# Kernel tuning notes

Measured on AMD Instinct MI355X. Metric: run time of the kernel, lower is better.

## Reference

```python
import jax, jax.numpy as jnp
import numpy as np

DIM = 256; Hh = 64; Ww = 64; L = Hh * Ww; B = 2
DIN = DIM          # expand = 1
DST = 16           # d_state
DTR = 16           # dt_rank = ceil(dim/16)
DCONV = 4


def _ln(x, g, b, eps=1e-5):
    m = jnp.mean(x, -1, keepdims=True)
    v = jnp.mean((x - m) ** 2, -1, keepdims=True)
    return (x - m) / jnp.sqrt(v + eps) * g + b


def _scan_dir(x, ep, z, convW, convb, xpW, dtW, dtb, A_log, Dp):
    # x, ep, z: (B, d_inner, L)
    xc = jnp.pad(x, ((0, 0), (0, 0), (DCONV - 1, 0)))  # causal depthwise conv
    xc = jax.lax.conv_general_dilated(
        xc, convW[:, None, :], (1,), 'VALID',
        feature_group_count=DIN, dimension_numbers=('NCH', 'OIH', 'NCH'))
    xs = jax.nn.silu(xc + convb[None, :, None])
    # cross: dt, B, C come from the OTHER modality's embedding (v7 cross-SSM)
    xdbl = jnp.einsum('bdl,kd->bkl', ep, xpW)               # (B, DTR+2N, L)
    dt = jax.nn.softplus(jnp.einsum('brl,dr->bdl', xdbl[:, :DTR], dtW) + dtb[None, :, None])
    Bm = xdbl[:, DTR:DTR + DST]                             # (B, N, L)
    Cm = xdbl[:, DTR + DST:]                                # (B, N, L)
    A = -jnp.exp(A_log)                                     # (d, N)
    dA = jnp.exp(jnp.einsum('bdl,dn->bdln', dt, A))         # (B, d, L, N)
    dBx = jnp.einsum('bdl,bnl,bdl->bdln', dt, Bm, xs)
    def comb(c1, c2):
        a1, b1 = c1; a2, b2 = c2
        return a1 * a2, a2 * b1 + b2
    _, h = jax.lax.associative_scan(comb, (dA, dBx), axis=2)  # h_l = dA_l h_{l-1} + dBx_l
    y = jnp.einsum('bdln,bnl->bdl', h, Cm) + Dp[None, :, None] * xs
    return y * jax.nn.silu(z)


def _mamba(u, e, in_proj_W, extra_proj_W,
           convf_W, convf_b, xprojf_W, dtf_W, dtf_b, A_log_f, D_f,
           convb_W, convb_b, xprojb_W, dtb_W, dtb_b, A_log_b, D_b,
           outnorm_g, outnorm_b, out_proj_W):
    xz = u @ in_proj_W.T                                    # (B, L, 2*d_inner)
    x = xz[..., :DIN].transpose(0, 2, 1)                    # (B, d, L)
    z = xz[..., DIN:].transpose(0, 2, 1)
    ep = (e @ extra_proj_W.T).transpose(0, 2, 1)            # (B, d, L)
    yf = _scan_dir(x, ep, z, convf_W, convf_b, xprojf_W, dtf_W, dtf_b, A_log_f, D_f)
    yb = jnp.flip(_scan_dir(jnp.flip(x, -1), jnp.flip(ep, -1), jnp.flip(z, -1),
                            convb_W, convb_b, xprojb_W, dtb_W, dtb_b, A_log_b, D_b), -1)
    y = (yf + yb) * 0.5                                     # if_devide_out
    y = _ln(y.transpose(0, 2, 1), outnorm_g, outnorm_b)     # use_norm
    return y @ out_proj_W.T


def setup_inputs() -> dict:
    key = jax.random.key(0)
    ks = jax.random.split(key, 20)
    s = 0.05
    dt_bias = float(np.log(np.expm1(0.01)))
    inp = {
        'input0': jax.random.normal(ks[0], (B, L, DIM), jnp.float32),
        'input1': jax.random.normal(ks[1], (B, L, DIM), jnp.float32),
        'norm0_g': jnp.ones((DIM,), jnp.float32), 'norm0_b': jnp.zeros((DIM,), jnp.float32),
        'norm1_g': jnp.ones((DIM,), jnp.float32), 'norm1_b': jnp.zeros((DIM,), jnp.float32),
        'cw_W': jax.random.normal(ks[2], (DIM, 2 * DIM), jnp.float32) * s,
        'cw_b': jnp.zeros((DIM,), jnp.float32),
        'in_proj_W': jax.random.normal(ks[3], (2 * DIN, DIM), jnp.float32) * s,
        'extra_proj_W': jax.random.normal(ks[4], (DIN, DIM), jnp.float32) * s,
        'convf_W': jax.random.normal(ks[5], (DIN, DCONV), jnp.float32) * 0.3,
        'convf_b': jnp.zeros((DIN,), jnp.float32),
        'xprojf_W': jax.random.normal(ks[6], (DTR + 2 * DST, DIN), jnp.float32) * s,
        'dtf_W': jax.random.normal(ks[7], (DIN, DTR), jnp.float32) * s,
        'dtf_b': jnp.full((DIN,), dt_bias, jnp.float32),
        'A_log_f': jnp.broadcast_to(jnp.log(jnp.arange(1, DST + 1, dtype=jnp.float32)), (DIN, DST)).copy(),
        'D_f': jnp.ones((DIN,), jnp.float32),
        'convb_W': jax.random.normal(ks[8], (DIN, DCONV), jnp.float32) * 0.3,
        'convb_b': jnp.zeros((DIN,), jnp.float32),
        'xprojb_W': jax.random.normal(ks[9], (DTR + 2 * DST, DIN), jnp.float32) * s,
        'dtb_W': jax.random.normal(ks[10], (DIN, DTR), jnp.float32) * s,
        'dtb_b': jnp.full((DIN,), dt_bias, jnp.float32),
        'A_log_b': jnp.broadcast_to(jnp.log(jnp.arange(1, DST + 1, dtype=jnp.float32)), (DIN, DST)).copy(),
        'D_b': jnp.ones((DIN,), jnp.float32),
        'outnorm_g': jnp.ones((DIN,), jnp.float32), 'outnorm_b': jnp.zeros((DIN,), jnp.float32),
        'out_proj_W': jax.random.normal(ks[11], (DIM, DIN), jnp.float32) * s,
        'post_g': jnp.ones((DIM,), jnp.float32), 'post_b': jnp.zeros((DIM,), jnp.float32),
    }
    return inp


def reference(input0, input1, norm0_g, norm0_b, norm1_g, norm1_b, cw_W, cw_b,
              in_proj_W, extra_proj_W,
              convf_W, convf_b, xprojf_W, dtf_W, dtf_b, A_log_f, D_f,
              convb_W, convb_b, xprojb_W, dtb_W, dtb_b, A_log_b, D_b,
              outnorm_g, outnorm_b, out_proj_W, post_g, post_b):
    skip = input0
    x0 = _ln(input0, norm0_g, norm0_b)
    x1 = _ln(input1, norm1_g, norm1_b)
    w = jax.nn.sigmoid(jnp.concatenate([x0, x1], -1) @ cw_W.T + cw_b)
    out = _mamba(x0, x1, in_proj_W, extra_proj_W,
                 convf_W, convf_b, xprojf_W, dtf_W, dtf_b, A_log_f, D_f,
                 convb_W, convb_b, xprojb_W, dtb_W, dtb_b, A_log_b, D_b,
                 outnorm_g, outnorm_b, out_proj_W)
    out = _ln(out, post_g, post_b)
    out = out * w + x0 * (1 - w)
    return out + skip
```

## Files before the change

kernel.cpp:

```cpp
#include <hip/hip_runtime.h>
#include <cstddef>

#define LL 4096
#define BB 2
#define DD 256
#define NEL ((size_t)BB * LL * DD)

typedef __bf16 bf16x8 __attribute__((ext_vector_type(8)));
typedef float f32x4 __attribute__((ext_vector_type(4)));
typedef unsigned short u16;

__device__ __forceinline__ float4 ld4(const float* p) { return *reinterpret_cast<const float4*>(p); }
__device__ __forceinline__ void st4(float* p, const float4 v) { *reinterpret_cast<float4*>(p) = v; }
__device__ __forceinline__ float softplusf(float x) { return fmaxf(x, 0.f) + log1pf(expf(-fabsf(x))); }
__device__ __forceinline__ u16 f2b(float f) {
    union { float f; unsigned u; } v; v.f = f;
    unsigned u = v.u;
    return (u16)((u + 0x7fffu + ((u >> 16) & 1u)) >> 16);
}

__device__ __forceinline__ void load16(const float* __restrict__ p, int fwd, float* dst) {
    if (fwd) {
#pragma unroll
        for (int k = 0; k < 4; ++k) {
            float4 v = ld4(p + 4 * k);
            dst[4 * k] = v.x; dst[4 * k + 1] = v.y; dst[4 * k + 2] = v.z; dst[4 * k + 3] = v.w;
        }
    } else {
#pragma unroll
        for (int k = 0; k < 4; ++k) {
            float4 v = ld4(p + 4 * k);
            dst[15 - 4 * k] = v.x; dst[14 - 4 * k] = v.y; dst[13 - 4 * k] = v.z; dst[12 - 4 * k] = v.w;
        }
    }
}

__device__ __forceinline__ void load16s(const float* __restrict__ row, int t, float* dst) {
#pragma unroll
    for (int s4 = 0; s4 < 4; ++s4) {
        float4 v = ld4(row + s4 * 1024 + t * 4);
        dst[4 * s4] = v.x; dst[4 * s4 + 1] = v.y; dst[4 * s4 + 2] = v.z; dst[4 * s4 + 3] = v.w;
    }
}


__global__ __launch_bounds__(256) void prep_q(
    const float* __restrict__ xpf, const float* __restrict__ xpb,
    const float* __restrict__ extW, float* __restrict__ Q, u16* __restrict__ wsH)
{
    const int r = blockIdx.x % 48;
    const int dir = blockIdx.x / 48;
    const int k = threadIdx.x;
    const float* xp = dir ? xpb : xpf;
    float s = 0.f;
    for (int n = 0; n < 256; ++n) s = fmaf(xp[r * 256 + n], extW[n * 256 + k], s);
    if (r < 16) Q[(dir * 16 + r) * 256 + k] = s;
    else        wsH[393216 + ((dir ? 32 : 0) + (r - 16)) * 256 + k] = f2b(s);
}

__global__ __launch_bounds__(256) void prep_w(
    const float* __restrict__ inW, const float* __restrict__ cwW,
    const float* __restrict__ outW, const float* __restrict__ dtfW,
    const float* __restrict__ dtbW, const float* __restrict__ Q,
    u16* __restrict__ wsH)
{
    const int idx = blockIdx.x * 256 + threadIdx.x;
    if (idx < 131072) {
        wsH[idx] = f2b(inW[idx]);
    } else if (idx < 262144) {
        wsH[idx] = f2b(cwW[idx - 131072]);
    } else if (idx < 393216) {
        const int i = idx - 262144;
        const int dir = i >> 16;
        const int j = i & 65535;
        const int n = j >> 8, k = j & 255;
        const float* dtW = dir ? dtbW : dtfW;
        const float* Qd = Q + dir * 4096;
        float s = 0.f;
#pragma unroll
        for (int r = 0; r < 16; ++r) s = fmaf(dtW[n * 16 + r], Qd[r * 256 + k], s);
        wsH[idx] = f2b(s);
    } else if (idx >= 409600 && idx < 475136) {
        wsH[idx] = f2b(outW[idx - 409600]);
    }
}

__global__ __launch_bounds__(64) void ln_rows(
    const float* __restrict__ in, float* __restrict__ outf, u16* __restrict__ outh,
    const float* __restrict__ g, const float* __restrict__ bb)
{
    const int row = blockIdx.x;
    const int t = threadIdx.x;
    const size_t off = (size_t)row * 256 + t * 4;
    float4 v = ld4(&in[off]);
    float s = v.x + v.y + v.z + v.w;
    float s2 = v.x * v.x + v.y * v.y + v.z * v.z + v.w * v.w;
#pragma unroll
    for (int dl = 1; dl < 64; dl <<= 1) { s += __shfl_xor(s, dl); s2 += __shfl_xor(s2, dl); }
    const float m = s * (1.f / 256.f);
    const float var = s2 * (1.f / 256.f) - m * m;
    const float rstd = rsqrtf(var + 1e-5f);
    const float4 gv = ld4(&g[t * 4]);
    const float4 bv = ld4(&bb[t * 4]);
    float4 r;
    r.x = (v.x - m) * rstd * gv.x + bv.x;
    r.y = (v.y - m) * rstd * gv.y + bv.y;
    r.z = (v.z - m) * rstd * gv.z + bv.z;
    r.w = (v.w - m) * rstd * gv.w + bv.w;
    if (outf) st4(&outf[off], r);
    ushort4 h; h.x = f2b(r.x); h.y = f2b(r.y); h.z = f2b(r.z); h.w = f2b(r.w);
    *reinterpret_cast<ushort4*>(&outh[off]) = h;
}

__global__ __launch_bounds__(256) void gemm_mfma(
    const u16* __restrict__ x0h, const u16* __restrict__ x1h, const u16* __restrict__ wsH,
    const float* __restrict__ cwb, const float* __restrict__ dtfb, const float* __restrict__ dtbb,
    float* __restrict__ xT, float* __restrict__ zT, float* __restrict__ wbuf,
    float* __restrict__ dtfT, float* __restrict__ dtbT,
    float* __restrict__ bcfT, float* __restrict__ bcbT)
{
    __shared__ __align__(16) u16 Blds[64 * 256];
    const int t = threadIdx.x;
    const int lane = t & 63;
    const int wid = t >> 6;
    const int col = lane & 15;
    const int kq = lane >> 4;
    const int m0 = blockIdx.x * 128;
    const int by = blockIdx.y;

    int seg, nbase, ldk, nhalf; const u16* W;
    if (by < 4)       { seg = 0; W = wsH + (size_t)(by * 64) * 256;                 ldk = 256; nhalf = 1; nbase = by * 64; }
    else if (by < 8)  { seg = 1; W = wsH + (size_t)(by * 64) * 256;                 ldk = 256; nhalf = 1; nbase = (by - 4) * 64; }
    else if (by < 12) { seg = 2; W = wsH + 131072 + (size_t)((by - 8) * 64) * 512;  ldk = 512; nhalf = 2; nbase = (by - 8) * 64; }
    else if (by < 16) { seg = 3; W = wsH + 262144 + (size_t)((by - 12) * 64) * 256; ldk = 256; nhalf = 1; nbase = (by - 12) * 64; }
    else if (by < 20) { seg = 4; W = wsH + 327680 + (size_t)((by - 16) * 64) * 256; ldk = 256; nhalf = 1; nbase = (by - 16) * 64; }
    else              { seg = 5; W = wsH + 393216;                                  ldk = 256; nhalf = 1; nbase = 0; }

    const u16* A0 = (seg >= 3) ? x1h : x0h;
    const int arow = m0 + wid * 32 + col;

    f32x4 acc[2][4] = {};
    for (int half = 0; half < nhalf; ++half) {
        if (half) __syncthreads();
#pragma unroll
        for (int it = 0; it < 8; ++it) {
            const int c = it * 256 + t;
            const int row = c >> 5, kc = c & 31;
            const bf16x8 v = *reinterpret_cast<const bf16x8*>(W + (size_t)row * ldk + half * 256 + kc * 8);
            const unsigned byt = ((unsigned)(row * 512 + kc * 16)) ^ (((unsigned)row & 7u) << 4);
            *reinterpret_cast<bf16x8*>(reinterpret_cast<char*>(Blds) + byt) = v;
        }
        __syncthreads();
        const u16* Ap = (seg == 2 && half) ? x1h : A0;
        const u16* Abase = Ap + (size_t)arow * 256;
        for (int k0 = 0; k0 < 256; k0 += 32) {
            const int kk = k0 + kq * 8;
            const bf16x8 a0 = *reinterpret_cast<const bf16x8*>(Abase + kk);
            const bf16x8 a1 = *reinterpret_cast<const bf16x8*>(Abase + 16 * 256 + kk);
#pragma unroll
            for (int nf = 0; nf < 4; ++nf) {
                const int n = nf * 16 + col;
                const unsigned byt = ((unsigned)(n * 512 + k0 * 2 + kq * 16)) ^ (((unsigned)n & 7u) << 4);
                const bf16x8 bfr = *reinterpret_cast<const bf16x8*>(reinterpret_cast<const char*>(Blds) + byt);
                acc[0][nf] = __builtin_amdgcn_mfma_f32_16x16x32_bf16(a0, bfr, acc[0][nf], 0, 0, 0);
                acc[1][nf] = __builtin_amdgcn_mfma_f32_16x16x32_bf16(a1, bfr, acc[1][nf], 0, 0, 0);
            }
        }
    }

    const int bb2 = m0 >> 12;
    const int l0 = m0 & (LL - 1);

    if (seg == 0 || seg == 1) {
        float* dst = (seg == 0) ? xT : zT;
#pragma unroll
        for (int rg = 0; rg < 2; ++rg) {
            const int mrow = wid * 32 + rg * 16 + kq * 4;
#pragma unroll
            for (int nf = 0; nf < 4; ++nf) {
                const int d = nbase + nf * 16 + col;
                *reinterpret_cast<f32x4*>(&dst[((size_t)bb2 * DD + d) * LL + l0 + mrow]) = acc[rg][nf];
            }
        }
    } else if (seg == 2) {
#pragma unroll
        for (int rg = 0; rg < 2; ++rg) {
            const int mrow = wid * 32 + rg * 16 + kq * 4;
#pragma unroll
            for (int nf = 0; nf < 4; ++nf) {
                const int n = nbase + nf * 16 + col;
                const float bv = cwb[n];
#pragma unroll
                for (int r = 0; r < 4; ++r)
                    wbuf[(size_t)(m0 + mrow + r) * 256 + n] = 1.f / (1.f + expf(-(acc[rg][nf][r] + bv)));
            }
        }
    } else if (seg == 3 || seg == 4) {
        const float* bias = (seg == 3) ? dtfb : dtbb;
        float* dst = (seg == 3) ? dtfT : dtbT;
#pragma unroll
        for (int rg = 0; rg < 2; ++rg) {
            const int tt = (l0 >> 4) + wid * 2 + rg;
#pragma unroll
            for (int nf = 0; nf < 4; ++nf) {
                const int d = nbase + nf * 16 + col;
                const float bv = bias[d];
                f32x4 o;
#pragma unroll
                for (int r = 0; r < 4; ++r) o[r] = softplusf(acc[rg][nf][r] + bv);
                const size_t rowb = ((size_t)bb2 * DD + d) * LL;
                if (seg == 3) {
                    *reinterpret_cast<f32x4*>(&dst[rowb + kq * 1024 + tt * 4]) = o;
                } else {
                    f32x4 orv = { o[3], o[2], o[1], o[0] };
                    *reinterpret_cast<f32x4*>(&dst[rowb + (3 - kq) * 1024 + (255 - tt) * 4]) = orv;
                }
            }
        }
    } else {
#pragma unroll
        for (int rg = 0; rg < 2; ++rg) {
            const int tt = (l0 >> 4) + wid * 2 + rg;
#pragma unroll
            for (int nf = 0; nf < 4; ++nf) {
                const int n = nf * 16 + col;
                const int comp = n & 31;
                if (n < 32) {
                    const size_t rowb = ((size_t)bb2 * 32 + comp) * LL;
                    *reinterpret_cast<f32x4*>(&bcfT[rowb + kq * 1024 + tt * 4]) = acc[rg][nf];
                } else {
                    const f32x4 a = acc[rg][nf];
                    f32x4 arv = { a[3], a[2], a[1], a[0] };
                    const size_t rowb = ((size_t)bb2 * 32 + comp) * LL;
                    *reinterpret_cast<f32x4*>(&bcbT[rowb + (3 - kq) * 1024 + (255 - tt) * 4]) = arv;
                }
            }
        }
    }
}

__global__ __launch_bounds__(256) void gemm_out_mfma(
    const u16* __restrict__ ynh, const u16* __restrict__ wsH, float* __restrict__ out)
{
    __shared__ __align__(16) u16 Blds[64 * 256];
    const int t = threadIdx.x;
    const int lane = t & 63;
    const int wid = t >> 6;
    const int col = lane & 15;
    const int kq = lane >> 4;
    const int m0 = blockIdx.x * 128;
    const int n0 = blockIdx.y * 64;
    const u16* W = wsH + 409600 + (size_t)n0 * 256;
    const int arow = m0 + wid * 32 + col;

#pragma unroll
    for (int it = 0; it < 8; ++it) {
        const int c = it * 256 + t;
        const int row = c >> 5, kc = c & 31;
        const bf16x8 v = *reinterpret_cast<const bf16x8*>(W + (size_t)row * 256 + kc * 8);
        const unsigned byt = ((unsigned)(row * 512 + kc * 16)) ^ (((unsigned)row & 7u) << 4);
        *reinterpret_cast<bf16x8*>(reinterpret_cast<char*>(Blds) + byt) = v;
    }
    __syncthreads();

    f32x4 acc[2][4] = {};
    const u16* Abase = ynh + (size_t)arow * 256;
    for (int k0 = 0; k0 < 256; k0 += 32) {
        const int kk = k0 + kq * 8;
        const bf16x8 a0 = *reinterpret_cast<const bf16x8*>(Abase + kk);
        const bf16x8 a1 = *reinterpret_cast<const bf16x8*>(Abase + 16 * 256 + kk);
#pragma unroll
        for (int nf = 0; nf < 4; ++nf) {
            const int n = nf * 16 + col;
            const unsigned byt = ((unsigned)(n * 512 + k0 * 2 + kq * 16)) ^ (((unsigned)n & 7u) << 4);
            const bf16x8 bfr = *reinterpret_cast<const bf16x8*>(reinterpret_cast<const char*>(Blds) + byt);
            acc[0][nf] = __builtin_amdgcn_mfma_f32_16x16x32_bf16(a0, bfr, acc[0][nf], 0, 0, 0);
            acc[1][nf] = __builtin_amdgcn_mfma_f32_16x16x32_bf16(a1, bfr, acc[1][nf], 0, 0, 0);
        }
    }
#pragma unroll
    for (int rg = 0; rg < 2; ++rg) {
        const int mrow = wid * 32 + rg * 16 + kq * 4;
#pragma unroll
        for (int nf = 0; nf < 4; ++nf) {
            const int n = n0 + nf * 16 + col;
#pragma unroll
            for (int r = 0; r < 4; ++r)
                out[(size_t)(m0 + mrow + r) * 256 + n] = acc[rg][nf][r];
        }
    }
}

__global__ __launch_bounds__(256) void scan_kernel(
    const float* __restrict__ xT, const float* __restrict__ zT,
    const float* __restrict__ dtfT, const float* __restrict__ dtbT,
    const float* __restrict__ bcfT, const float* __restrict__ bcbT,
    const float* __restrict__ cfW, const float* __restrict__ cfB,
    const float* __restrict__ cbW, const float* __restrict__ cbB,
    const float* __restrict__ AlF, const float* __restrict__ AlB,
    const float* __restrict__ DF, const float* __restrict__ DB,
    float* __restrict__ yF, float* __restrict__ yB)
{
    const int d = blockIdx.x;
    const int b = blockIdx.y;
    const int dir = blockIdx.z;
    const int t = threadIdx.x;
    const int lane = t & 63;
    const int wv = t >> 6;
    const int fwd = (dir == 0);
    const float* dtT = fwd ? dtfT : dtbT;
    const float* bcT = fwd ? bcfT : bcbT;
    const float* cW  = fwd ? cfW  : cbW;
    const float* cBv = fwd ? cfB  : cbB;
    const float* Al  = fwd ? AlF  : AlB;
    const float* Dp  = fwd ? DF   : DB;
    float* yout = fwd ? yF : yB;

    const int p0 = t * 16;
    const size_t xbase = ((size_t)b * DD + d) * LL;
    const int ls = LL - 16 - p0;
    const int off16 = fwd ? p0 : ls;

    const float Dd = Dp[d];
    const float c0 = cW[d * 4 + 0], c1 = cW[d * 4 + 1], c2 = cW[d * 4 + 2], c3 = cW[d * 4 + 3];
    const float cbias = cBv[d];

    float xq[19];
    if (fwd) {
#pragma unroll
        for (int k = 0; k < 4; ++k) {
            float4 v = ld4(&xT[xbase + p0 + 4 * k]);
            xq[3 + 4 * k] = v.x; xq[4 + 4 * k] = v.y; xq[5 + 4 * k] = v.z; xq[6 + 4 * k] = v.w;
        }
        xq[2] = (p0 >= 1) ? xT[xbase + p0 - 1] : 0.f;
        xq[1] = (p0 >= 2) ? xT[xbase + p0 - 2] : 0.f;
        xq[0] = (p0 >= 3) ? xT[xbase + p0 - 3] : 0.f;
    } else {
#pragma unroll
        for (int k = 0; k < 4; ++k) {
            float4 v = ld4(&xT[xbase + ls + 4 * k]);
            xq[18 - 4 * k] = v.x; xq[17 - 4 * k] = v.y; xq[16 - 4 * k] = v.z; xq[15 - 4 * k] = v.w;
        }
        xq[2] = (p0 >= 1) ? xT[xbase + LL - p0] : 0.f;
        xq[1] = (p0 >= 2) ? xT[xbase + LL + 1 - p0] : 0.f;
        xq[0] = (p0 >= 3) ? xT[xbase + LL + 2 - p0] : 0.f;
    }

    float dt[16];
    load16s(dtT + xbase, t, dt);

    float dtxs[16], yacc[16];
#pragma unroll
    for (int s = 0; s < 16; ++s) {
        float c = fmaf(xq[s], c0, fmaf(xq[s + 1], c1, fmaf(xq[s + 2], c2, fmaf(xq[s + 3], c3, cbias))));
        const float xv = c / (1.f + expf(-c));
        dtxs[s] = dt[s] * xv;
        yacc[s] = Dd * xv;
    }

    const float* bcb0 = bcT + (size_t)b * 32 * LL;

    __shared__ float wPs[2][4];
    __shared__ float wSs[2][4];

#pragma unroll 1
    for (int n = 0; n < 16; ++n) {
        const float a2 = -expf(Al[d * 16 + n]) * 1.4426950408889634f;
        float Bn[16];
        load16s(bcb0 + (size_t)n * LL, t, Bn);
        float pw[16], hl[16];
        float Pl = 1.f, Sl = 0.f;
#pragma unroll
        for (int s = 0; s < 16; ++s) {
            const float w = exp2f(dt[s] * a2);
            Sl = fmaf(w, Sl, dtxs[s] * Bn[s]);
            Pl *= w;
            pw[s] = Pl; hl[s] = Sl;
        }
        float Cn[16];
        load16s(bcb0 + (size_t)(16 + n) * LL, t, Cn);
#pragma unroll
        for (int dl = 1; dl < 64; dl <<= 1) {
            const float Pp = __shfl_up(Pl, dl);
            const float Sp = __shfl_up(Sl, dl);
            if (lane >= dl) { Sl = fmaf(Pl, Sp, Sl); Pl *= Pp; }
        }
        const int buf = n & 1;
        if (lane == 63) { wPs[buf][wv] = Pl; wSs[buf][wv] = Sl; }
        __syncthreads();
        float WSv = 0.f;
#pragma unroll
        for (int w2 = 0; w2 < 3; ++w2)
            if (w2 < wv) WSv = fmaf(wPs[buf][w2], WSv, wSs[buf][w2]);
        const float Pex = __shfl_up(Pl, 1);
        const float Sex = __shfl_up(Sl, 1);
        const float hin = lane ? fmaf(Pex, WSv, Sex) : WSv;
#pragma unroll
        for (int s = 0; s < 16; ++s)
            yacc[s] = fmaf(fmaf(pw[s], hin, hl[s]), Cn[s], yacc[s]);
    }

    float zq[16];
    load16(&zT[xbase + off16], fwd, zq);
    float yv[16];
#pragma unroll
    for (int s = 0; s < 16; ++s) {
        const float zz = zq[s];
        yv[s] = yacc[s] * zz / (1.f + expf(-zz));
    }

    if (fwd) {
#pragma unroll
        for (int k = 0; k < 4; ++k)
            st4(&yout[xbase + p0 + 4 * k], make_float4(yv[4 * k], yv[4 * k + 1], yv[4 * k + 2], yv[4 * k + 3]));
    } else {
#pragma unroll
        for (int k = 0; k < 4; ++k)
            st4(&yout[xbase + ls + 4 * k], make_float4(yv[15 - 4 * k], yv[14 - 4 * k], yv[13 - 4 * k], yv[12 - 4 * k]));
    }
}

__global__ __launch_bounds__(256) void comb_ln(
    const float* __restrict__ yF, const float* __restrict__ yB,
    const float* __restrict__ g, const float* __restrict__ bb,
    u16* __restrict__ out)
{
    __shared__ float tile[256][33];
    __shared__ float rs[8][32];
    __shared__ float rs2[8][32];
    const int b = blockIdx.y;
    const int l0 = blockIdx.x * 32;
    const int t = threadIdx.x;
    {
        const size_t base = ((size_t)b * DD + t) * LL + l0;
#pragma unroll
        for (int k = 0; k < 8; ++k) {
            float4 f = ld4(&yF[base + 4 * k]);
            float4 bv = ld4(&yB[base + 4 * k]);
            tile[t][4 * k + 0] = (f.x + bv.x) * 0.5f;
            tile[t][4 * k + 1] = (f.y + bv.y) * 0.5f;
            tile[t][4 * k + 2] = (f.z + bv.z) * 0.5f;
            tile[t][4 * k + 3] = (f.w + bv.w) * 0.5f;
        }
    }
    __syncthreads();
    const int l = t & 31;
    const int grp = t >> 5;
    float s = 0.f, s2 = 0.f;
#pragma unroll
    for (int i = 0; i < 32; ++i) {
        const float v = tile[grp * 32 + i][l];
        s += v; s2 = fmaf(v, v, s2);
    }
    rs[grp][l] = s; rs2[grp][l] = s2;
    __syncthreads();
    float st = 0.f, st2 = 0.f;
#pragma unroll
    for (int gq = 0; gq < 8; ++gq) { st += rs[gq][l]; st2 += rs2[gq][l]; }
    const float m = st * (1.f / 256.f);
    const float var = st2 * (1.f / 256.f) - m * m;
    const float rstd = rsqrtf(var + 1e-5f);
    const size_t obase = ((size_t)b * LL + l0 + l) * 256 + grp * 32;
#pragma unroll
    for (int k = 0; k < 8; ++k) {
        const float4 gv = ld4(&g[grp * 32 + 4 * k]);
        const float4 bv2 = ld4(&bb[grp * 32 + 4 * k]);
        ushort4 h;
        h.x = f2b((tile[grp * 32 + 4 * k + 0][l] - m) * rstd * gv.x + bv2.x);
        h.y = f2b((tile[grp * 32 + 4 * k + 1][l] - m) * rstd * gv.y + bv2.y);
        h.z = f2b((tile[grp * 32 + 4 * k + 2][l] - m) * rstd * gv.z + bv2.z);
        h.w = f2b((tile[grp * 32 + 4 * k + 3][l] - m) * rstd * gv.w + bv2.w);
        *reinterpret_cast<ushort4*>(&out[obase + 4 * k]) = h;
    }
}

__global__ __launch_bounds__(64) void final_kernel(
    const float* __restrict__ o, const float* __restrict__ w,
    const float* __restrict__ x0n, const float* __restrict__ in0,
    const float* __restrict__ pg, const float* __restrict__ pb,
    float* __restrict__ outp)
{
    const int row = blockIdx.x;
    const int t = threadIdx.x;
    const size_t off = (size_t)row * 256 + t * 4;
    float4 v = ld4(&o[off]);
    float s = v.x + v.y + v.z + v.w;
    float s2 = v.x * v.x + v.y * v.y + v.z * v.z + v.w * v.w;
#pragma unroll
    for (int dl = 1; dl < 64; dl <<= 1) { s += __shfl_xor(s, dl); s2 += __shfl_xor(s2, dl); }
    const float m = s * (1.f / 256.f);
    const float var = s2 * (1.f / 256.f) - m * m;
    const float rstd = rsqrtf(var + 1e-5f);
    const float4 gv = ld4(&pg[t * 4]);
    const float4 bv = ld4(&pb[t * 4]);
    const float4 wv = ld4(&w[off]);
    const float4 xv = ld4(&x0n[off]);
    const float4 iv = ld4(&in0[off]);
    float4 r;
    r.x = ((v.x - m) * rstd * gv.x + bv.x) * wv.x + xv.x * (1.f - wv.x) + iv.x;
    r.y = ((v.y - m) * rstd * gv.y + bv.y) * wv.y + xv.y * (1.f - wv.y) + iv.y;
    r.z = ((v.z - m) * rstd * gv.z + bv.z) * wv.z + xv.z * (1.f - wv.z) + iv.z;
    r.w = ((v.w - m) * rstd * gv.w + bv.w) * wv.w + xv.w * (1.f - wv.w) + iv.w;
    st4(&outp[off], r);
}

extern "C" void kernel_launch(void* const* d_in, const int* in_sizes, int n_in,
                              void* d_out, int out_size, void* d_ws, size_t ws_size,
                              hipStream_t stream) {
    (void)in_sizes; (void)n_in; (void)out_size; (void)ws_size;
    const float* in0      = (const float*)d_in[0];
    const float* in1      = (const float*)d_in[1];
    const float* norm0_g  = (const float*)d_in[2];
    const float* norm0_b  = (const float*)d_in[3];
    const float* norm1_g  = (const float*)d_in[4];
    const float* norm1_b  = (const float*)d_in[5];
    const float* cw_W     = (const float*)d_in[6];
    const float* cw_b     = (const float*)d_in[7];
    const float* in_proj_W    = (const float*)d_in[8];
    const float* extra_proj_W = (const float*)d_in[9];
    const float* convf_W  = (const float*)d_in[10];
    const float* convf_b  = (const float*)d_in[11];
    const float* xprojf_W = (const float*)d_in[12];
    const float* dtf_W    = (const float*)d_in[13];
    const float* dtf_b    = (const float*)d_in[14];
    const float* A_log_f  = (const float*)d_in[15];
    const float* D_f      = (const float*)d_in[16];
    const float* convb_W  = (const float*)d_in[17];
    const float* convb_b  = (const float*)d_in[18];
    const float* xprojb_W = (const float*)d_in[19];
    const float* dtb_W    = (const float*)d_in[20];
    const float* dtb_b    = (const float*)d_in[21];
    const float* A_log_b  = (const float*)d_in[22];
    const float* D_b      = (const float*)d_in[23];
    const float* outnorm_g = (const float*)d_in[24];
    const float* outnorm_b = (const float*)d_in[25];
    const float* out_proj_W = (const float*)d_in[26];
    const float* post_g   = (const float*)d_in[27];
    const float* post_b   = (const float*)d_in[28];

    float* ws = (float*)d_ws;
    float* x0n   = ws;
    float* xT    = ws + NEL;
    float* zT    = ws + 2 * NEL;
    float* dtfT  = ws + 3 * NEL;
    float* dtbT  = ws + 4 * NEL;
    float* wbuf  = ws + 5 * NEL;
    float* yF    = ws + 6 * NEL;
    float* yB    = ws + 7 * NEL;
    float* bcfT  = ws + 8 * NEL;
    float* bcbT  = bcfT + (size_t)BB * 32 * LL;
    u16*   wsH   = (u16*)(bcbT + (size_t)BB * 32 * LL);
    float* Qtmp  = (float*)(wsH + 475136);

    u16* x0h = (u16*)yF;
    u16* x1h = x0h + NEL;
    u16* ynormh = (u16*)dtfT;
    float* obuf = dtbT;

    prep_q<<<96, 256, 0, stream>>>(xprojf_W, xprojb_W, extra_proj_W, Qtmp, wsH);
    prep_w<<<1856, 256, 0, stream>>>(in_proj_W, cw_W, out_proj_W, dtf_W, dtb_W, Qtmp, wsH);
    ln_rows<<<BB * LL, 64, 0, stream>>>(in0, x0n, x0h, norm0_g, norm0_b);
    ln_rows<<<BB * LL, 64, 0, stream>>>(in1, nullptr, x1h, norm1_g, norm1_b);
    gemm_mfma<<<dim3(64, 21, 1), 256, 0, stream>>>(x0h, x1h, wsH, cw_b, dtf_b, dtb_b,
                                                   xT, zT, wbuf, dtfT, dtbT, bcfT, bcbT);
    scan_kernel<<<dim3(256, 2, 2), 256, 0, stream>>>(xT, zT, dtfT, dtbT, bcfT, bcbT,
                                                     convf_W, convf_b, convb_W, convb_b,
                                                     A_log_f, A_log_b, D_f, D_b,
                                                     yF, yB);
    comb_ln<<<dim3(128, 2, 1), 256, 0, stream>>>(yF, yB, outnorm_g, outnorm_b, ynormh);
    gemm_out_mfma<<<dim3(64, 4, 1), 256, 0, stream>>>(ynormh, wsH, obuf);
    final_kernel<<<BB * LL, 64, 0, stream>>>(obuf, wbuf, x0n, in0, post_g, post_b, (float*)d_out);
}
```

Measured before the change: 125.1 us.

## Split scan sequence across 512 threads with 8 elements per thread

The selective-scan kernel now runs 512 threads per block, each handling 8 sequence positions instead of 16. The permuted dt/B/C loads are remapped so each thread takes half of its former owner's chunk, and the cross-wave carry combine is extended from 4 to 8 waves. The goal is a shorter per-thread serial recurrence, fewer registers per thread and more parallelism to hide latency. In exchange, each block does more shuffle-scan and cross-wave combine work.

```diff
diff --git a/kernel.cpp b/kernel.cpp
--- a/kernel.cpp
+++ b/kernel.cpp
@@ -35,11 +35,13 @@
     }
 }
 
-__device__ __forceinline__ void load16s(const float* __restrict__ row, int t, float* dst) {
-#pragma unroll
-    for (int s4 = 0; s4 < 4; ++s4) {
-        float4 v = ld4(row + s4 * 1024 + t * 4);
-        dst[4 * s4] = v.x; dst[4 * s4 + 1] = v.y; dst[4 * s4 + 2] = v.z; dst[4 * s4 + 3] = v.w;
+__device__ __forceinline__ void load8s(const float* __restrict__ row, int t, float* dst) {
+    const int tt = t >> 1;
+    const int s4b = (t & 1) * 2;
+#pragma unroll
+    for (int q = 0; q < 2; ++q) {
+        float4 v = ld4(row + (s4b + q) * 1024 + tt * 4);
+        dst[4 * q] = v.x; dst[4 * q + 1] = v.y; dst[4 * q + 2] = v.z; dst[4 * q + 3] = v.w;
     }
 }
 
@@ -291,7 +293,7 @@
     }
 }
 
-__global__ __launch_bounds__(256) void scan_kernel(
+__global__ __launch_bounds__(512) void scan_kernel(
     const float* __restrict__ xT, const float* __restrict__ zT,
     const float* __restrict__ dtfT, const float* __restrict__ dtbT,
     const float* __restrict__ bcfT, const float* __restrict__ bcbT,
@@ -316,19 +318,18 @@
     const float* Dp  = fwd ? DF   : DB;
     float* yout = fwd ? yF : yB;
 
-    const int p0 = t * 16;
+    const int p0 = t * 8;
     const size_t xbase = ((size_t)b * DD + d) * LL;
-    const int ls = LL - 16 - p0;
-    const int off16 = fwd ? p0 : ls;
+    const int ls = LL - 8 - p0;
 
     const float Dd = Dp[d];
     const float c0 = cW[d * 4 + 0], c1 = cW[d * 4 + 1], c2 = cW[d * 4 + 2], c3 = cW[d * 4 + 3];
     const float cbias = cBv[d];
 
-    float xq[19];
+    float xq[11];
     if (fwd) {
 #pragma unroll
-        for (int k = 0; k < 4; ++k) {
+        for (int k = 0; k < 2; ++k) {
             float4 v = ld4(&xT[xbase + p0 + 4 * k]);
             xq[3 + 4 * k] = v.x; xq[4 + 4 * k] = v.y; xq[5 + 4 * k] = v.z; xq[6 + 4 * k] = v.w;
         }
@@ -337,21 +338,21 @@
         xq[0] = (p0 >= 3) ? xT[xbase + p0 - 3] : 0.f;
     } else {
 #pragma unroll
-        for (int k = 0; k < 4; ++k) {
+        for (int k = 0; k < 2; ++k) {
             float4 v = ld4(&xT[xbase + ls + 4 * k]);
-            xq[18 - 4 * k] = v.x; xq[17 - 4 * k] = v.y; xq[16 - 4 * k] = v.z; xq[15 - 4 * k] = v.w;
+            xq[10 - 4 * k] = v.x; xq[9 - 4 * k] = v.y; xq[8 - 4 * k] = v.z; xq[7 - 4 * k] = v.w;
         }
         xq[2] = (p0 >= 1) ? xT[xbase + LL - p0] : 0.f;
         xq[1] = (p0 >= 2) ? xT[xbase + LL + 1 - p0] : 0.f;
         xq[0] = (p0 >= 3) ? xT[xbase + LL + 2 - p0] : 0.f;
     }
 
-    float dt[16];
-    load16s(dtT + xbase, t, dt);
-
-    float dtxs[16], yacc[16];
-#pragma unroll
-    for (int s = 0; s < 16; ++s) {
+    float dt[8];
+    load8s(dtT + xbase, t, dt);
+
+    float dtxs[8], yacc[8];
+#pragma unroll
+    for (int s = 0; s < 8; ++s) {
         float c = fmaf(xq[s], c0, fmaf(xq[s + 1], c1, fmaf(xq[s + 2], c2, fmaf(xq[s + 3], c3, cbias))));
         const float xv = c / (1.f + expf(-c));
         dtxs[s] = dt[s] * xv;
@@ -360,25 +361,25 @@
 
     const float* bcb0 = bcT + (size_t)b * 32 * LL;
 
-    __shared__ float wPs[2][4];
-    __shared__ float wSs[2][4];
+    __shared__ float wPs[2][8];
+    __shared__ float wSs[2][8];
 
 #pragma unroll 1
     for (int n = 0; n < 16; ++n) {
         const float a2 = -expf(Al[d * 16 + n]) * 1.4426950408889634f;
-        float Bn[16];
-        load16s(bcb0 + (size_t)n * LL, t, Bn);
-        float pw[16], hl[16];
+        float Bn[8];
+        load8s(bcb0 + (size_t)n * LL, t, Bn);
+        float pw[8], hl[8];
         float Pl = 1.f, Sl = 0.f;
 #pragma unroll
-        for (int s = 0; s < 16; ++s) {
+        for (int s = 0; s < 8; ++s) {
             const float w = exp2f(dt[s] * a2);
             Sl = fmaf(w, Sl, dtxs[s] * Bn[s]);
             Pl *= w;
             pw[s] = Pl; hl[s] = Sl;
         }
-        float Cn[16];
-        load16s(bcb0 + (size_t)(16 + n) * LL, t, Cn);
+        float Cn[8];
+        load8s(bcb0 + (size_t)(16 + n) * LL, t, Cn);
 #pragma unroll
         for (int dl = 1; dl < 64; dl <<= 1) {
             const float Pp = __shfl_up(Pl, dl);
@@ -390,33 +391,45 @@
         __syncthreads();
         float WSv = 0.f;
 #pragma unroll
-        for (int w2 = 0; w2 < 3; ++w2)
+        for (int w2 = 0; w2 < 7; ++w2)
             if (w2 < wv) WSv = fmaf(wPs[buf][w2], WSv, wSs[buf][w2]);
         const float Pex = __shfl_up(Pl, 1);
         const float Sex = __shfl_up(Sl, 1);
         const float hin = lane ? fmaf(Pex, WSv, Sex) : WSv;
 #pragma unroll
-        for (int s = 0; s < 16; ++s)
+        for (int s = 0; s < 8; ++s)
             yacc[s] = fmaf(fmaf(pw[s], hin, hl[s]), Cn[s], yacc[s]);
     }
 
-    float zq[16];
-    load16(&zT[xbase + off16], fwd, zq);
-    float yv[16];
-#pragma unroll
-    for (int s = 0; s < 16; ++s) {
+    float zq[8];
+    if (fwd) {
+#pragma unroll
+        for (int k = 0; k < 2; ++k) {
+            float4 v = ld4(&zT[xbase + p0 + 4 * k]);
+            zq[4 * k] = v.x; zq[4 * k + 1] = v.y; zq[4 * k + 2] = v.z; zq[4 * k + 3] = v.w;
+        }
+    } else {
+#pragma unroll
+        for (int k = 0; k < 2; ++k) {
+            float4 v = ld4(&zT[xbase + ls + 4 * k]);
+            zq[7 - 4 * k] = v.x; zq[6 - 4 * k] = v.y; zq[5 - 4 * k] = v.z; zq[4 - 4 * k] = v.w;
+        }
+    }
+    float yv[8];
+#pragma unroll
+    for (int s = 0; s < 8; ++s) {
         const float zz = zq[s];
         yv[s] = yacc[s] * zz / (1.f + expf(-zz));
     }
 
     if (fwd) {
 #pragma unroll
-        for (int k = 0; k < 4; ++k)
+        for (int k = 0; k < 2; ++k)
             st4(&yout[xbase + p0 + 4 * k], make_float4(yv[4 * k], yv[4 * k + 1], yv[4 * k + 2], yv[4 * k + 3]));
     } else {
 #pragma unroll
-        for (int k = 0; k < 4; ++k)
-            st4(&yout[xbase + ls + 4 * k], make_float4(yv[15 - 4 * k], yv[14 - 4 * k], yv[13 - 4 * k], yv[12 - 4 * k]));
+        for (int k = 0; k < 2; ++k)
+            st4(&yout[xbase + ls + 4 * k], make_float4(yv[7 - 4 * k], yv[6 - 4 * k], yv[5 - 4 * k], yv[4 - 4 * k]));
     }
 }
 
@@ -563,7 +576,7 @@
     ln_rows<<<BB * LL, 64, 0, stream>>>(in1, nullptr, x1h, norm1_g, norm1_b);
     gemm_mfma<<<dim3(64, 21, 1), 256, 0, stream>>>(x0h, x1h, wsH, cw_b, dtf_b, dtb_b,
                                                    xT, zT, wbuf, dtfT, dtbT, bcfT, bcbT);
-    scan_kernel<<<dim3(256, 2, 2), 256, 0, stream>>>(xT, zT, dtfT, dtbT, bcfT, bcbT,
+    scan_kernel<<<dim3(256, 2, 2), 512, 0, stream>>>(xT, zT, dtfT, dtbT, bcfT, bcbT,
                                                      convf_W, convf_b, convb_W, convb_b,
                                                      A_log_f, A_log_b, D_f, D_b,
                                                      yF, yB);
```

New measurement: 133.8 us. 1.07x slower.

## Store x, z and scan outputs in bf16; fuse LN launches and recompute x0 norm

Applied to the files above, without the earlier changes.

The x and z projections and the forward/backward scan outputs are now stored as bf16 instead of fp32, which halves the intermediate traffic between the GEMM, the scan and comb_ln. The two layernorm launches are merged into one kernel. The fp32 x0 normalised buffer is no longer written; the final kernel recomputes LN(input0) instead. The C-row load in the scan is hoisted next to the B load. Lower precision in x, z and y adds rounding error in exchange for less memory traffic.

```diff
diff --git a/kernel.cpp b/kernel.cpp
--- a/kernel.cpp
+++ b/kernel.cpp
@@ -18,20 +18,29 @@
     unsigned u = v.u;
     return (u16)((u + 0x7fffu + ((u >> 16) & 1u)) >> 16);
 }
-
-__device__ __forceinline__ void load16(const float* __restrict__ p, int fwd, float* dst) {
+__device__ __forceinline__ float b2f(unsigned bits16) {
+    union { unsigned u; float f; } v; v.u = bits16 << 16; return v.f;
+}
+
+__device__ __forceinline__ void load16h(const u16* __restrict__ p, int fwd, float* dst) {
+    const uint4 a = *reinterpret_cast<const uint4*>(p);
+    const uint4 c = *reinterpret_cast<const uint4*>(p + 8);
+    const unsigned* au = reinterpret_cast<const unsigned*>(&a);
+    const unsigned* cu = reinterpret_cast<const unsigned*>(&c);
+    float tmp[16];
+#pragma unroll
+    for (int j = 0; j < 4; ++j) {
+        tmp[2 * j]     = b2f(au[j] & 0xffffu);
+        tmp[2 * j + 1] = b2f(au[j] >> 16);
+        tmp[8 + 2 * j]     = b2f(cu[j] & 0xffffu);
+        tmp[8 + 2 * j + 1] = b2f(cu[j] >> 16);
+    }
     if (fwd) {
 #pragma unroll
-        for (int k = 0; k < 4; ++k) {
-            float4 v = ld4(p + 4 * k);
-            dst[4 * k] = v.x; dst[4 * k + 1] = v.y; dst[4 * k + 2] = v.z; dst[4 * k + 3] = v.w;
-        }
+        for (int s = 0; s < 16; ++s) dst[s] = tmp[s];
     } else {
 #pragma unroll
-        for (int k = 0; k < 4; ++k) {
-            float4 v = ld4(p + 4 * k);
-            dst[15 - 4 * k] = v.x; dst[14 - 4 * k] = v.y; dst[13 - 4 * k] = v.z; dst[12 - 4 * k] = v.w;
-        }
+        for (int s = 0; s < 16; ++s) dst[s] = tmp[15 - s];
     }
 }
 
@@ -85,11 +94,18 @@
     }
 }
 
-__global__ __launch_bounds__(64) void ln_rows(
-    const float* __restrict__ in, float* __restrict__ outf, u16* __restrict__ outh,
-    const float* __restrict__ g, const float* __restrict__ bb)
-{
-    const int row = blockIdx.x;
+__global__ __launch_bounds__(64) void ln_rows2(
+    const float* __restrict__ in0, const float* __restrict__ in1,
+    const float* __restrict__ g0, const float* __restrict__ b0,
+    const float* __restrict__ g1, const float* __restrict__ b1,
+    u16* __restrict__ x0h, u16* __restrict__ x1h)
+{
+    const int which = blockIdx.x >> 13;
+    const int row = blockIdx.x & 8191;
+    const float* in = which ? in1 : in0;
+    const float* g  = which ? g1 : g0;
+    const float* bb = which ? b1 : b0;
+    u16* outh = which ? x1h : x0h;
     const int t = threadIdx.x;
     const size_t off = (size_t)row * 256 + t * 4;
     float4 v = ld4(&in[off]);
@@ -102,20 +118,18 @@
     const float rstd = rsqrtf(var + 1e-5f);
     const float4 gv = ld4(&g[t * 4]);
     const float4 bv = ld4(&bb[t * 4]);
-    float4 r;
-    r.x = (v.x - m) * rstd * gv.x + bv.x;
-    r.y = (v.y - m) * rstd * gv.y + bv.y;
-    r.z = (v.z - m) * rstd * gv.z + bv.z;
-    r.w = (v.w - m) * rstd * gv.w + bv.w;
-    if (outf) st4(&outf[off], r);
-    ushort4 h; h.x = f2b(r.x); h.y = f2b(r.y); h.z = f2b(r.z); h.w = f2b(r.w);
+    ushort4 h;
+    h.x = f2b((v.x - m) * rstd * gv.x + bv.x);
+    h.y = f2b((v.y - m) * rstd * gv.y + bv.y);
+    h.z = f2b((v.z - m) * rstd * gv.z + bv.z);
+    h.w = f2b((v.w - m) * rstd * gv.w + bv.w);
     *reinterpret_cast<ushort4*>(&outh[off]) = h;
 }
 
 __global__ __launch_bounds__(256) void gemm_mfma(
     const u16* __restrict__ x0h, const u16* __restrict__ x1h, const u16* __restrict__ wsH,
     const float* __restrict__ cwb, const float* __restrict__ dtfb, const float* __restrict__ dtbb,
-    float* __restrict__ xT, float* __restrict__ zT, float* __restrict__ wbuf,
+    u16* __restrict__ xTh, u16* __restrict__ zTh, float* __restrict__ wbuf,
     float* __restrict__ dtfT, float* __restrict__ dtbT,
     float* __restrict__ bcfT, float* __restrict__ bcbT)
 {
@@ -172,14 +186,17 @@
     const int l0 = m0 & (LL - 1);
 
     if (seg == 0 || seg == 1) {
-        float* dst = (seg == 0) ? xT : zT;
+        u16* dst = (seg == 0) ? xTh : zTh;
 #pragma unroll
         for (int rg = 0; rg < 2; ++rg) {
             const int mrow = wid * 32 + rg * 16 + kq * 4;
 #pragma unroll
             for (int nf = 0; nf < 4; ++nf) {
                 const int d = nbase + nf * 16 + col;
-                *reinterpret_cast<f32x4*>(&dst[((size_t)bb2 * DD + d) * LL + l0 + mrow]) = acc[rg][nf];
+                ushort4 h;
+                h.x = f2b(acc[rg][nf][0]); h.y = f2b(acc[rg][nf][1]);
+                h.z = f2b(acc[rg][nf][2]); h.w = f2b(acc[rg][nf][3]);
+                *reinterpret_cast<ushort4*>(&dst[((size_t)bb2 * DD + d) * LL + l0 + mrow]) = h;
             }
         }
     } else if (seg == 2) {
@@ -292,14 +309,14 @@
 }
 
 __global__ __launch_bounds__(256) void scan_kernel(
-    const float* __restrict__ xT, const float* __restrict__ zT,
+    const u16* __restrict__ xTh, const u16* __restrict__ zTh,
     const float* __restrict__ dtfT, const float* __restrict__ dtbT,
     const float* __restrict__ bcfT, const float* __restrict__ bcbT,
     const float* __restrict__ cfW, const float* __restrict__ cfB,
     const float* __restrict__ cbW, const float* __restrict__ cbB,
     const float* __restrict__ AlF, const float* __restrict__ AlB,
     const float* __restrict__ DF, const float* __restrict__ DB,
-    float* __restrict__ yF, float* __restrict__ yB)
+    u16* __restrict__ yFh, u16* __restrict__ yBh)
 {
     const int d = blockIdx.x;
     const int b = blockIdx.y;
@@ -314,7 +331,7 @@
     const float* cBv = fwd ? cfB  : cbB;
     const float* Al  = fwd ? AlF  : AlB;
     const float* Dp  = fwd ? DF   : DB;
-    float* yout = fwd ? yF : yB;
+    u16* yout = fwd ? yFh : yBh;
 
     const int p0 = t * 16;
     const size_t xbase = ((size_t)b * DD + d) * LL;
@@ -326,24 +343,15 @@
     const float cbias = cBv[d];
 
     float xq[19];
+    load16h(&xTh[xbase + off16], fwd, xq + 3);
     if (fwd) {
-#pragma unroll
-        for (int k = 0; k < 4; ++k) {
-            float4 v = ld4(&xT[xbase + p0 + 4 * k]);
-            xq[3 + 4 * k] = v.x; xq[4 + 4 * k] = v.y; xq[5 + 4 * k] = v.z; xq[6 + 4 * k] = v.w;
-        }
-        xq[2] = (p0 >= 1) ? xT[xbase + p0 - 1] : 0.f;
-        xq[1] = (p0 >= 2) ? xT[xbase + p0 - 2] : 0.f;
-        xq[0] = (p0 >= 3) ? xT[xbase + p0 - 3] : 0.f;
+        xq[2] = (p0 >= 1) ? b2f(xTh[xbase + p0 - 1]) : 0.f;
+        xq[1] = (p0 >= 2) ? b2f(xTh[xbase + p0 - 2]) : 0.f;
+        xq[0] = (p0 >= 3) ? b2f(xTh[xbase + p0 - 3]) : 0.f;
     } else {
-#pragma unroll
-        for (int k = 0; k < 4; ++k) {
-            float4 v = ld4(&xT[xbase + ls + 4 * k]);
-            xq[18 - 4 * k] = v.x; xq[17 - 4 * k] = v.y; xq[16 - 4 * k] = v.z; xq[15 - 4 * k] = v.w;
-        }
-        xq[2] = (p0 >= 1) ? xT[xbase + LL - p0] : 0.f;
-        xq[1] = (p0 >= 2) ? xT[xbase + LL + 1 - p0] : 0.f;
-        xq[0] = (p0 >= 3) ? xT[xbase + LL + 2 - p0] : 0.f;
+        xq[2] = (p0 >= 1) ? b2f(xTh[xbase + LL - p0]) : 0.f;
+        xq[1] = (p0 >= 2) ? b2f(xTh[xbase + LL + 1 - p0]) : 0.f;
+        xq[0] = (p0 >= 3) ? b2f(xTh[xbase + LL + 2 - p0]) : 0.f;
     }
 
     float dt[16];
@@ -366,8 +374,9 @@
 #pragma unroll 1
     for (int n = 0; n < 16; ++n) {
         const float a2 = -expf(Al[d * 16 + n]) * 1.4426950408889634f;
-        float Bn[16];
+        float Bn[16], Cn[16];
         load16s(bcb0 + (size_t)n * LL, t, Bn);
+        load16s(bcb0 + (size_t)(16 + n) * LL, t, Cn);
         float pw[16], hl[16];
         float Pl = 1.f, Sl = 0.f;
 #pragma unroll
@@ -377,8 +386,6 @@
             Pl *= w;
             pw[s] = Pl; hl[s] = Sl;
         }
-        float Cn[16];
-        load16s(bcb0 + (size_t)(16 + n) * LL, t, Cn);
 #pragma unroll
         for (int dl = 1; dl < 64; dl <<= 1) {
             const float Pp = __shfl_up(Pl, dl);
@@ -401,7 +408,7 @@
     }
 
     float zq[16];
-    load16(&zT[xbase + off16], fwd, zq);
+    load16h(&zTh[xbase + off16], fwd, zq);
     float yv[16];
 #pragma unroll
     for (int s = 0; s < 16; ++s) {
@@ -409,19 +416,26 @@
         yv[s] = yacc[s] * zz / (1.f + expf(-zz));
     }
 
-    if (fwd) {
-#pragma unroll
-        for (int k = 0; k < 4; ++k)
-            st4(&yout[xbase + p0 + 4 * k], make_float4(yv[4 * k], yv[4 * k + 1], yv[4 * k + 2], yv[4 * k + 3]));
-    } else {
-#pragma unroll
-        for (int k = 0; k < 4; ++k)
-            st4(&yout[xbase + ls + 4 * k], make_float4(yv[15 - 4 * k], yv[14 - 4 * k], yv[13 - 4 * k], yv[12 - 4 * k]));
+#pragma unroll
+    for (int g = 0; g < 2; ++g) {
+        uint4 U;
+        unsigned* up = reinterpret_cast<unsigned*>(&U);
+        if (fwd) {
+#pragma unroll
+            for (int j = 0; j < 4; ++j)
+                up[j] = (unsigned)f2b(yv[8 * g + 2 * j]) | ((unsigned)f2b(yv[8 * g + 2 * j + 1]) << 16);
+            *reinterpret_cast<uint4*>(&yout[xbase + p0 + 8 * g]) = U;
+        } else {
+#pragma unroll
+            for (int j = 0; j < 4; ++j)
+                up[j] = (unsigned)f2b(yv[15 - 8 * g - 2 * j]) | ((unsigned)f2b(yv[15 - 8 * g - 2 * j - 1]) << 16);
+            *reinterpret_cast<uint4*>(&yout[xbase + ls + 8 * g]) = U;
+        }
     }
 }
 
 __global__ __launch_bounds__(256) void comb_ln(
-    const float* __restrict__ yF, const float* __restrict__ yB,
+    const u16* __restrict__ yFh, const u16* __restrict__ yBh,
     const float* __restrict__ g, const float* __restrict__ bb,
     u16* __restrict__ out)
 {
@@ -434,13 +448,16 @@
     {
         const size_t base = ((size_t)b * DD + t) * LL + l0;
 #pragma unroll
-        for (int k = 0; k < 8; ++k) {
-            float4 f = ld4(&yF[base + 4 * k]);
-            float4 bv = ld4(&yB[base + 4 * k]);
-            tile[t][4 * k + 0] = (f.x + bv.x) * 0.5f;
-            tile[t][4 * k + 1] = (f.y + bv.y) * 0.5f;
-            tile[t][4 * k + 2] = (f.z + bv.z) * 0.5f;
-            tile[t][4 * k + 3] = (f.w + bv.w) * 0.5f;
+        for (int k = 0; k < 4; ++k) {
+            const uint4 fa = *reinterpret_cast<const uint4*>(&yFh[base + 8 * k]);
+            const uint4 ba = *reinterpret_cast<const uint4*>(&yBh[base + 8 * k]);
+            const unsigned* fu = reinterpret_cast<const unsigned*>(&fa);
+            const unsigned* bu = reinterpret_cast<const unsigned*>(&ba);
+#pragma unroll
+            for (int j = 0; j < 4; ++j) {
+                tile[t][8 * k + 2 * j]     = (b2f(fu[j] & 0xffffu) + b2f(bu[j] & 0xffffu)) * 0.5f;
+                tile[t][8 * k + 2 * j + 1] = (b2f(fu[j] >> 16) + b2f(bu[j] >> 16)) * 0.5f;
+            }
         }
     }
     __syncthreads();
@@ -476,7 +493,8 @@
 
 __global__ __launch_bounds__(64) void final_kernel(
     const float* __restrict__ o, const float* __restrict__ w,
-    const float* __restrict__ x0n, const float* __restrict__ in0,
+    const float* __restrict__ in0,
+    const float* __restrict__ n0g, const float* __restrict__ n0b,
     const float* __restrict__ pg, const float* __restrict__ pb,
     float* __restrict__ outp)
 {
@@ -484,23 +502,34 @@
     const int t = threadIdx.x;
     const size_t off = (size_t)row * 256 + t * 4;
     float4 v = ld4(&o[off]);
+    float4 iv = ld4(&in0[off]);
     float s = v.x + v.y + v.z + v.w;
     float s2 = v.x * v.x + v.y * v.y + v.z * v.z + v.w * v.w;
-#pragma unroll
-    for (int dl = 1; dl < 64; dl <<= 1) { s += __shfl_xor(s, dl); s2 += __shfl_xor(s2, dl); }
+    float si = iv.x + iv.y + iv.z + iv.w;
+    float si2 = iv.x * iv.x + iv.y * iv.y + iv.z * iv.z + iv.w * iv.w;
+#pragma unroll
+    for (int dl = 1; dl < 64; dl <<= 1) {
+        s += __shfl_xor(s, dl); s2 += __shfl_xor(s2, dl);
+        si += __shfl_xor(si, dl); si2 += __shfl_xor(si2, dl);
+    }
     const float m = s * (1.f / 256.f);
-    const float var = s2 * (1.f / 256.f) - m * m;
-    const float rstd = rsqrtf(var + 1e-5f);
+    const float rstd = rsqrtf(s2 * (1.f / 256.f) - m * m + 1e-5f);
+    const float mi = si * (1.f / 256.f);
+    const float rstdi = rsqrtf(si2 * (1.f / 256.f) - mi * mi + 1e-5f);
     const float4 gv = ld4(&pg[t * 4]);
     const float4 bv = ld4(&pb[t * 4]);
+    const float4 g0 = ld4(&n0g[t * 4]);
+    const float4 b0 = ld4(&n0b[t * 4]);
     const float4 wv = ld4(&w[off]);
-    const float4 xv = ld4(&x0n[off]);
-    const float4 iv = ld4(&in0[off]);
     float4 r;
-    r.x = ((v.x - m) * rstd * gv.x + bv.x) * wv.x + xv.x * (1.f - wv.x) + iv.x;
-    r.y = ((v.y - m) * rstd * gv.y + bv.y) * wv.y + xv.y * (1.f - wv.y) + iv.y;
-    r.z = ((v.z - m) * rstd * gv.z + bv.z) * wv.z + xv.z * (1.f - wv.z) + iv.z;
-    r.w = ((v.w - m) * rstd * gv.w + bv.w) * wv.w + xv.w * (1.f - wv.w) + iv.w;
+    const float x0x = (iv.x - mi) * rstdi * g0.x + b0.x;
+    const float x0y = (iv.y - mi) * rstdi * g0.y + b0.y;
+    const float x0z = (iv.z - mi) * rstdi * g0.z + b0.z;
+    const float x0w = (iv.w - mi) * rstdi * g0.w + b0.w;
+    r.x = ((v.x - m) * rstd * gv.x + bv.x) * wv.x + x0x * (1.f - wv.x) + iv.x;
+    r.y = ((v.y - m) * rstd * gv.y + bv.y) * wv.y + x0y * (1.f - wv.y) + iv.y;
+    r.z = ((v.z - m) * rstd * gv.z + bv.z) * wv.z + x0z * (1.f - wv.z) + iv.z;
+    r.w = ((v.w - m) * rstd * gv.w + bv.w) * wv.w + x0w * (1.f - wv.w) + iv.w;
     st4(&outp[off], r);
 }
 
@@ -539,35 +568,38 @@
     const float* post_b   = (const float*)d_in[28];
 
     float* ws = (float*)d_ws;
-    float* x0n   = ws;
-    float* xT    = ws + NEL;
-    float* zT    = ws + 2 * NEL;
-    float* dtfT  = ws + 3 * NEL;
-    float* dtbT  = ws + 4 * NEL;
-    float* wbuf  = ws + 5 * NEL;
-    float* yF    = ws + 6 * NEL;
-    float* yB    = ws + 7 * NEL;
-    float* bcfT  = ws + 8 * NEL;
+    float* xzr   = ws;
+    float* dtfT  = ws + NEL;
+    float* dtbT  = ws + 2 * NEL;
+    float* wbuf  = ws + 3 * NEL;
+    float* yFr   = ws + 4 * NEL;
+    float* yBr   = ws + 5 * NEL;
+    float* bcfT  = ws + 6 * NEL;
     float* bcbT  = bcfT + (size_t)BB * 32 * LL;
     u16*   wsH   = (u16*)(bcbT + (size_t)BB * 32 * LL);
     float* Qtmp  = (float*)(wsH + 475136);
 
-    u16* x0h = (u16*)yF;
+    u16* xTh = (u16*)xzr;
+    u16* zTh = xTh + NEL;
+    u16* x0h = (u16*)yFr;
     u16* x1h = x0h + NEL;
+    u16* yFh = (u16*)yFr;
+    u16* yBh = (u16*)yBr;
     u16* ynormh = (u16*)dtfT;
     float* obuf = dtbT;
 
     prep_q<<<96, 256, 0, stream>>>(xprojf_W, xprojb_W, extra_proj_W, Qtmp, wsH);
     prep_w<<<1856, 256, 0, stream>>>(in_proj_W, cw_W, out_proj_W, dtf_W, dtb_W, Qtmp, wsH);
-    ln_rows<<<BB * LL, 64, 0, stream>>>(in0, x0n, x0h, norm0_g, norm0_b);
-    ln_rows<<<BB * LL, 64, 0, stream>>>(in1, nullptr, x1h, norm1_g, norm1_b);
+    ln_rows2<<<2 * BB * LL, 64, 0, stream>>>(in0, in1, norm0_g, norm0_b, norm1_g, norm1_b,
+                                             x0h, x1h);
     gemm_mfma<<<dim3(64, 21, 1), 256, 0, stream>>>(x0h, x1h, wsH, cw_b, dtf_b, dtb_b,
-                                                   xT, zT, wbuf, dtfT, dtbT, bcfT, bcbT);
-    scan_kernel<<<dim3(256, 2, 2), 256, 0, stream>>>(xT, zT, dtfT, dtbT, bcfT, bcbT,
+                                                   xTh, zTh, wbuf, dtfT, dtbT, bcfT, bcbT);
+    scan_kernel<<<dim3(256, 2, 2), 256, 0, stream>>>(xTh, zTh, dtfT, dtbT, bcfT, bcbT,
                                                      convf_W, convf_b, convb_W, convb_b,
                                                      A_log_f, A_log_b, D_f, D_b,
-                                                     yF, yB);
-    comb_ln<<<dim3(128, 2, 1), 256, 0, stream>>>(yF, yB, outnorm_g, outnorm_b, ynormh);
+                                                     yFh, yBh);
+    comb_ln<<<dim3(128, 2, 1), 256, 0, stream>>>(yFh, yBh, outnorm_g, outnorm_b, ynormh);
     gemm_out_mfma<<<dim3(64, 4, 1), 256, 0, stream>>>(ynormh, wsH, obuf);
-    final_kernel<<<BB * LL, 64, 0, stream>>>(obuf, wbuf, x0n, in0, post_g, post_b, (float*)d_out);
-}
+    final_kernel<<<BB * LL, 64, 0, stream>>>(obuf, wbuf, in0, norm0_g, norm0_b,
+                                             post_g, post_b, (float*)d_out);
+}
```

Measured after the change: 118.7 us. 1.05x faster.
